# Optimization experiments

Hardware: AMD Instinct MI355X
Metric: run time of the kernel (lower is better)

The kernel has to match this reference:

```python
import jax, jax.numpy as jnp
import numpy as np

B, N, C = 32, 128, 128
HE = 64                      # n_hidden_edge
FILTERS = [64, 256, 512]
K = 3
NREL = 2
NH = 256                     # n_hidden
OUT = 10
EPS_BN = 1e-5


def _lin(key, fin, fout):
    return jax.random.normal(key, (fin, fout), jnp.float32) / np.sqrt(fin)


def setup_inputs() -> dict:
    key = jax.random.key(0)
    ks = iter(jax.random.split(key, 64))
    x = jax.random.normal(next(ks), (B, N, C), jnp.float32)
    # ragged mask: first n_b nodes active
    n_nodes = jax.random.randint(next(ks), (B,), 64, N + 1)
    mask = (jnp.arange(N)[None, :] < n_nodes[:, None]).astype(jnp.float32)
    A = jax.random.uniform(next(ks), (B, N, N), jnp.float32)
    A = A * mask[:, :, None] * mask[:, None, :]
    inp = {"x": x, "A": A, "mask": mask}
    # edge predictor MLP: Linear(2C,HE) -> ReLU -> Linear(HE,1)
    inp["eW1"] = _lin(next(ks), 2 * C, HE)
    inp["eb1"] = jnp.zeros((HE,), jnp.float32)
    inp["eW2"] = _lin(next(ks), HE, 1)
    inp["eb2"] = jnp.zeros((1,), jnp.float32)
    # 3 GraphConv layers: fc (in*K*NREL -> f), BN eval params
    fin = C
    for li, f in enumerate(FILTERS):
        inp[f"gW{li}"] = _lin(next(ks), fin * K * NREL, f)
        inp[f"gb{li}"] = jnp.zeros((f,), jnp.float32)
        inp[f"g{li}g"] = jnp.ones((f,), jnp.float32)
        inp[f"g{li}b"] = jnp.zeros((f,), jnp.float32)
        inp[f"g{li}m"] = 0.1 * jax.random.normal(next(ks), (f,), jnp.float32)
        inp[f"g{li}v"] = jax.random.uniform(next(ks), (f,), jnp.float32) + 0.5
        fin = f
    # classifier fc (dropout is identity in eval)
    inp["fW1"] = _lin(next(ks), FILTERS[-1], NH)
    inp["fb1"] = jnp.zeros((NH,), jnp.float32)
    inp["fW2"] = _lin(next(ks), NH, OUT)
    inp["fb2"] = jnp.zeros((OUT,), jnp.float32)
    return inp


def _edge_adjacency(x, mask, eW1, eb1, eW2, eb2):
    # edge_pred(cat(x_i,x_j)) for all pairs; flipped pass == transpose of scores
    u = x @ eW1[:C]          # [B,N,HE] (contribution of node i slot)
    v = x @ eW1[C:]          # [B,N,HE] (contribution of node j slot)
    h = jax.nn.relu(u[:, :, None, :] + v[:, None, :, :] + eb1)   # [B,N,N,HE]
    s = jnp.einsum('bijh,h->bij', h, eW2[:, 0]) + eb2[0]          # [B,N,N]
    y = jnp.exp(0.5 * (s + jnp.swapaxes(s, 1, 2)))
    # only masked upper-triangular pairs (i<j) were scattered in the original
    tri = jnp.triu(jnp.ones((N, N), bool), 1)
    pm = tri[None, :, :] * (mask[:, :, None] * mask[:, None, :])
    A_pred = y * pm
    rs = jnp.sum(A_pred, axis=2)                                 # row sums (torch sum over dim 1 of [N,N])
    rs = jnp.where(rs == 0.0, 1.0, rs)
    An = A_pred / rs[:, :, None]
    return An + jnp.swapaxes(An, 1, 2)


def _gconv(xh, A2, mask, W, b, g, be, m, v):
    outs = []
    for rel in range(A2.shape[-1]):
        Ar = A2[..., rel]
        # K>=2, scale_identity=False -> no identity added
        D = (jnp.sum(Ar, axis=1) + 1e-5) ** (-0.5)               # [B,N]
        L = D[:, :, None] * Ar * D[:, None, :]
        Xt = [xh, jnp.matmul(L, xh)]
        for _ in range(2, K):
            Xt.append(2.0 * jnp.matmul(L, Xt[-1]) - Xt[-2])
        outs.append(jnp.concatenate(Xt, axis=2))
    h = jnp.concatenate(outs, axis=2) @ W + b
    h = h * mask[:, :, None]
    h = (h - m) / jnp.sqrt(v + EPS_BN) * g + be                  # BatchNorm1d eval over channel dim
    return jax.nn.relu(h)


def reference(x, A, mask, eW1, eb1, eW2, eb2,
              gW0, gb0, g0g, g0b, g0m, g0v,
              gW1, gb1, g1g, g1b, g1m, g1v,
              gW2, gb2, g2g, g2b, g2m, g2v,
              fW1, fb1, fW2, fb2):
    An = _edge_adjacency(x, mask, eW1, eb1, eW2, eb2)
    A2 = jnp.stack((A, An), axis=3)                              # [B,N,N,2]
    h = _gconv(x, A2, mask, gW0, gb0, g0g, g0b, g0m, g0v)
    h = _gconv(h, A2, mask, gW1, gb1, g1g, g1b, g1m, g1v)
    h = _gconv(h, A2, mask, gW2, gb2, g2g, g2b, g2m, g2v)
    pooled = jnp.max(h, axis=1)                                  # [B, 512]
    # fc: Dropout(eval=id) -> Linear -> Dropout(eval=id) -> Linear (no activation)
    return (pooled @ fW1 + fb1) @ fW2 + fb2
```

## Files before the change

### kernel.cpp

```cpp
#include <hip/hip_runtime.h>

#define Bk 32
#define Nn 128
#define Cc 128
#define HE 64
#define BN_EPS 1e-5f

typedef __attribute__((ext_vector_type(8))) short short8;
typedef __attribute__((ext_vector_type(4))) float floatx4;

#define OFF_U    ((size_t)0)
#define OFF_V    ((size_t)262144)
#define OFF_S    ((size_t)524288)
#define OFF_AN   ((size_t)1048576)
#define OFF_LB   ((size_t)1572864)
#define OFF_H0   ((size_t)2097152)
#define OFF_H1   ((size_t)2359296)
#define OFF_H2   ((size_t)3407872)
#define OFF_XB   ((size_t)5505024)
#define OFF_WT   ((size_t)8650752)

__device__ __forceinline__ unsigned short f2b(float f) {
    unsigned int x = __float_as_uint(f);
    unsigned int r = x + 0x7FFFu + ((x >> 16) & 1u);
    return (unsigned short)(r >> 16);
}

__global__ __launch_bounds__(128) void edge_uv(const float* __restrict__ x,
                                               const float* __restrict__ eW1,
                                               const float* __restrict__ eb1,
                                               float* __restrict__ u, float* __restrict__ v) {
    int bn = blockIdx.x;
    int tid = threadIdx.x;
    __shared__ float xs[Cc];
    xs[tid] = x[(size_t)bn * Cc + tid];
    __syncthreads();
    int h = tid & 63;
    int which = tid >> 6;
    const float* W = eW1 + (size_t)which * Cc * HE + h;
    float acc = 0.f;
#pragma unroll 8
    for (int c = 0; c < Cc; ++c) acc += xs[c] * W[(size_t)c * HE];
    if (which == 0) u[(size_t)bn * HE + h] = acc + eb1[h];
    else            v[(size_t)bn * HE + h] = acc;
}

__global__ __launch_bounds__(256) void edge_score(const float* __restrict__ u,
                                                  const float* __restrict__ v,
                                                  const float* __restrict__ eW2,
                                                  const float* __restrict__ eb2,
                                                  float* __restrict__ s) {
    __shared__ float us[16][68], vs[16][68], w2[HE];
    int b = blockIdx.z;
    int i0 = blockIdx.y * 16, j0 = blockIdx.x * 16;
    int tid = threadIdx.x;
    int r = tid >> 4, c4 = (tid & 15) * 4;
    {
        const float4 uv = *(const float4*)(u + ((size_t)(b * Nn + i0 + r)) * HE + c4);
        us[r][c4] = uv.x; us[r][c4 + 1] = uv.y; us[r][c4 + 2] = uv.z; us[r][c4 + 3] = uv.w;
        const float4 vv = *(const float4*)(v + ((size_t)(b * Nn + j0 + r)) * HE + c4);
        vs[r][c4] = vv.x; vs[r][c4 + 1] = vv.y; vs[r][c4 + 2] = vv.z; vs[r][c4 + 3] = vv.w;
    }
    if (tid < HE) w2[tid] = eW2[tid];
    __syncthreads();
    int il = tid >> 4, jl = tid & 15;
    float acc = 0.f;
#pragma unroll
    for (int h = 0; h < HE; ++h) {
        float t = us[il][h] + vs[jl][h];
        acc += fmaxf(t, 0.f) * w2[h];
    }
    s[((size_t)(b * Nn + i0 + il)) * Nn + j0 + jl] = acc + eb2[0];
}

__global__ __launch_bounds__(256) void edge_apan(const float* __restrict__ s,
                                                 const float* __restrict__ mask,
                                                 float* __restrict__ An) {
    __shared__ float apS[128][129];
    __shared__ float rsS[128];
    __shared__ float msk[128];
    int b = blockIdx.x, tid = threadIdx.x;
    const float* sb = s + (size_t)b * Nn * Nn;
    if (tid < 128) msk[tid] = mask[b * Nn + tid];
    __syncthreads();
#pragma unroll
    for (int k = 0; k < 64; ++k) {
        int idx = tid + k * 256;
        int i = idx >> 7, j = idx & 127;
        float val = 0.f;
        if (j > i && msk[i] != 0.f && msk[j] != 0.f) {
            val = expf(fminf(0.5f * (sb[idx] + sb[j * Nn + i]), 80.f));
        }
        apS[i][j] = val;
    }
    __syncthreads();
    if (tid < 128) {
        float r = 0.f;
        for (int j = 0; j < 128; ++j) r += apS[tid][j];
        rsS[tid] = (r == 0.f) ? 1.f : r;
    }
    __syncthreads();
    float* Ab = An + (size_t)b * Nn * Nn;
#pragma unroll
    for (int k = 0; k < 64; ++k) {
        int idx = tid + k * 256;
        int i = idx >> 7, j = idx & 127;
        Ab[idx] = apS[i][j] / rsS[i] + apS[j][i] / rsS[j];
    }
}

__global__ __launch_bounds__(256) void buildLb(const float* __restrict__ A,
                                               const float* __restrict__ An,
                                               unsigned short* __restrict__ Lb) {
    int b = blockIdx.x & 31, rel = blockIdx.x >> 5;
    const float* Ar = (rel ? An : A) + (size_t)b * Nn * Nn;
    __shared__ float part[256];
    __shared__ float Ds[128];
    int tid = threadIdx.x;
    int j = tid & 127, half = tid >> 7;
    float sum = 0.f;
    for (int i = half * 64; i < half * 64 + 64; ++i) sum += Ar[i * Nn + j];
    part[tid] = sum;
    __syncthreads();
    if (tid < 128) Ds[tid] = rsqrtf(part[tid] + part[tid + 128] + 1e-5f);
    __syncthreads();
    unsigned short* Lo = Lb + ((size_t)(rel * Bk + b)) * Nn * Nn;
#pragma unroll
    for (int k = 0; k < 64; ++k) {
        int idx = tid + k * 256;
        int i = idx >> 7, jj = idx & 127;
        Lo[idx] = f2b(Ds[i] * Ar[idx] * Ds[jj]);
    }
}

__global__ __launch_bounds__(256) void prep_weights(const float* __restrict__ W0,
                                                    const float* __restrict__ W1,
                                                    const float* __restrict__ W2,
                                                    unsigned short* __restrict__ Wt) {
    int e = blockIdx.x * 256 + threadIdx.x;
    if (e < 49152) {
        int k = e >> 6, n = e & 63;
        Wt[n * 768 + k] = f2b(W0[e]);
        return;
    }
    e -= 49152;
    if (e < 98304) {
        int k = e >> 8, n = e & 255;
        Wt[49152 + n * 384 + k] = f2b(W1[e]);
        return;
    }
    e -= 98304;
    if (e < 786432) {
        int k = e >> 9, n = e & 511;
        Wt[147456 + n * 1536 + k] = f2b(W2[e]);
    }
}

template <int FIN>
__global__ __launch_bounds__(256) void cheb_fused(const unsigned short* __restrict__ Lb,
                                                  const float* __restrict__ xin,
                                                  unsigned short* __restrict__ Xb) {
    constexpr int LDK = 136;
    __shared__ __align__(16) unsigned short Ls[128 * LDK];
    __shared__ __align__(16) unsigned short XsT[64 * LDK];
    __shared__ __align__(16) unsigned short T1T[64 * LDK];
    int z = blockIdx.y;
    int b = z & 31, rel = z >> 5;
    int c0 = blockIdx.x * 64;
    int tid = threadIdx.x;
    int w = tid >> 6, lane = tid & 63, quad = lane >> 4, lr = lane & 15;
    const unsigned short* Lp = Lb + ((size_t)(rel * Bk + b)) * Nn * Nn;
    const float* Xp = xin + (size_t)b * Nn * FIN;
    const int ld6 = 6 * FIN;
    unsigned short* Xo = Xb + (size_t)b * Nn * ld6 + rel * 3 * FIN;

#pragma unroll
    for (int i = 0; i < 16; ++i) {
        int idx = tid + i * 256;
        int row = idx >> 5, col4 = (idx & 31) << 2;
        ushort4 val = *(const ushort4*)(Lp + row * Nn + col4);
        *(ushort4*)&Ls[row * LDK + col4] = val;
    }
    {
        int node = tid >> 1, cb = (tid & 1) * 32;
        const float* xr = Xp + (size_t)node * FIN + c0 + cb;
        unsigned short* t0w = Xo + (size_t)node * ld6 + c0 + cb;
#pragma unroll
        for (int i = 0; i < 8; ++i) {
            float4 vv = *(const float4*)(xr + i * 4);
            ushort4 o;
            o.x = f2b(vv.x); o.y = f2b(vv.y); o.z = f2b(vv.z); o.w = f2b(vv.w);
            *(ushort4*)(t0w + i * 4) = o;
            XsT[(cb + i * 4 + 0) * LDK + node] = o.x;
            XsT[(cb + i * 4 + 1) * LDK + node] = o.y;
            XsT[(cb + i * 4 + 2) * LDK + node] = o.z;
            XsT[(cb + i * 4 + 3) * LDK + node] = o.w;
        }
    }
    __syncthreads();

    floatx4 acc[2][4];
#pragma unroll
    for (int rt = 0; rt < 2; ++rt)
#pragma unroll
        for (int ct = 0; ct < 4; ++ct) acc[rt][ct] = (floatx4){0.f, 0.f, 0.f, 0.f};
#pragma unroll
    for (int kc = 0; kc < 4; ++kc) {
        short8 a[2], bb[4];
#pragma unroll
        for (int rt = 0; rt < 2; ++rt)
            a[rt] = *(const short8*)&Ls[((w * 2 + rt) * 16 + lr) * LDK + kc * 32 + quad * 8];
#pragma unroll
        for (int ct = 0; ct < 4; ++ct)
            bb[ct] = *(const short8*)&XsT[(ct * 16 + lr) * LDK + kc * 32 + quad * 8];
#pragma unroll
        for (int rt = 0; rt < 2; ++rt)
#pragma unroll
            for (int ct = 0; ct < 4; ++ct)
                acc[rt][ct] = __builtin_amdgcn_mfma_f32_16x16x32_bf16(a[rt], bb[ct], acc[rt][ct], 0, 0, 0);
    }
#pragma unroll
    for (int rt = 0; rt < 2; ++rt) {
        int rb = (w * 2 + rt) * 16 + quad * 4;
#pragma unroll
        for (int ct = 0; ct < 4; ++ct) {
            int col = ct * 16 + lr;
            ushort4 o;
            o.x = f2b(acc[rt][ct][0]); o.y = f2b(acc[rt][ct][1]);
            o.z = f2b(acc[rt][ct][2]); o.w = f2b(acc[rt][ct][3]);
            *(ushort4*)&T1T[col * LDK + rb] = o;
        }
    }
    __syncthreads();

    {
        int node = tid >> 1, cb = (tid & 1) * 32;
        unsigned short* t1w = Xo + (size_t)node * ld6 + FIN + c0 + cb;
#pragma unroll
        for (int i = 0; i < 8; ++i) {
            ushort4 o;
            o.x = T1T[(cb + i * 4 + 0) * LDK + node];
            o.y = T1T[(cb + i * 4 + 1) * LDK + node];
            o.z = T1T[(cb + i * 4 + 2) * LDK + node];
            o.w = T1T[(cb + i * 4 + 3) * LDK + node];
            *(ushort4*)(t1w + i * 4) = o;
        }
    }
    floatx4 acc2[2][4];
#pragma unroll
    for (int rt = 0; rt < 2; ++rt)
#pragma unroll
        for (int ct = 0; ct < 4; ++ct) acc2[rt][ct] = (floatx4){0.f, 0.f, 0.f, 0.f};
#pragma unroll
    for (int kc = 0; kc < 4; ++kc) {
        short8 a[2], bb[4];
#pragma unroll
        for (int rt = 0; rt < 2; ++rt)
            a[rt] = *(const short8*)&Ls[((w * 2 + rt) * 16 + lr) * LDK + kc * 32 + quad * 8];
#pragma unroll
        for (int ct = 0; ct < 4; ++ct)
            bb[ct] = *(const short8*)&T1T[(ct * 16 + lr) * LDK + kc * 32 + quad * 8];
#pragma unroll
        for (int rt = 0; rt < 2; ++rt)
#pragma unroll
            for (int ct = 0; ct < 4; ++ct)
                acc2[rt][ct] = __builtin_amdgcn_mfma_f32_16x16x32_bf16(a[rt], bb[ct], acc2[rt][ct], 0, 0, 0);
    }
#pragma unroll
    for (int rt = 0; rt < 2; ++rt) {
        int rb = (w * 2 + rt) * 16 + quad * 4;
#pragma unroll
        for (int ct = 0; ct < 4; ++ct) {
            int col = ct * 16 + lr;
            ushort4 o;
            float t0a = Xp[(size_t)(rb + 0) * FIN + c0 + col];
            float t0b = Xp[(size_t)(rb + 1) * FIN + c0 + col];
            float t0c = Xp[(size_t)(rb + 2) * FIN + c0 + col];
            float t0d = Xp[(size_t)(rb + 3) * FIN + c0 + col];
            o.x = f2b(2.f * acc2[rt][ct][0] - t0a);
            o.y = f2b(2.f * acc2[rt][ct][1] - t0b);
            o.z = f2b(2.f * acc2[rt][ct][2] - t0c);
            o.w = f2b(2.f * acc2[rt][ct][3] - t0d);
            *(ushort4*)&XsT[col * LDK + rb] = o;
        }
    }
    __syncthreads();
    {
        int node = tid >> 1, cb = (tid & 1) * 32;
        unsigned short* t2w = Xo + (size_t)node * ld6 + 2 * FIN + c0 + cb;
#pragma unroll
        for (int i = 0; i < 8; ++i) {
            ushort4 o;
            o.x = XsT[(cb + i * 4 + 0) * LDK + node];
            o.y = XsT[(cb + i * 4 + 1) * LDK + node];
            o.z = XsT[(cb + i * 4 + 2) * LDK + node];
            o.w = XsT[(cb + i * 4 + 3) * LDK + node];
            *(ushort4*)(t2w + i * 4) = o;
        }
    }
}

template <int RT>
__global__ __launch_bounds__(256) void fc_mfma(const unsigned short* __restrict__ Xb,
                                               const unsigned short* __restrict__ Wt,
                                               const float* __restrict__ bias,
                                               const float* __restrict__ mask,
                                               const float* __restrict__ bnG,
                                               const float* __restrict__ bnB,
                                               const float* __restrict__ bnM,
                                               const float* __restrict__ bnV,
                                               float* __restrict__ out, int Kd, int F) {
    __shared__ __align__(16) unsigned short As[RT * 64 * 40];
    __shared__ __align__(16) unsigned short Bs[64 * 40];
    int tid = threadIdx.x;
    int w = tid >> 6, lane = tid & 63, quad = lane >> 4, lr = lane & 15;
    int row0 = blockIdx.y * (RT * 64), col0 = blockIdx.x * 64;

    floatx4 acc[RT][4];
#pragma unroll
    for (int rt = 0; rt < RT; ++rt)
#pragma unroll
        for (int ct = 0; ct < 4; ++ct) acc[rt][ct] = (floatx4){0.f, 0.f, 0.f, 0.f};

    int arow[RT], asub[RT];
#pragma unroll
    for (int i = 0; i < RT; ++i) { int ch = tid + i * 256; arow[i] = ch >> 2; asub[i] = ch & 3; }
    int brow = tid >> 2, bsub = tid & 3;

    for (int k0 = 0; k0 < Kd; k0 += 32) {
        short8 ra[RT];
#pragma unroll
        for (int i = 0; i < RT; ++i)
            ra[i] = *(const short8*)(Xb + (size_t)(row0 + arow[i]) * Kd + k0 + asub[i] * 8);
        short8 rb = *(const short8*)(Wt + (size_t)(col0 + brow) * Kd + k0 + bsub * 8);
        __syncthreads();
#pragma unroll
        for (int i = 0; i < RT; ++i)
            *(short8*)&As[arow[i] * 40 + asub[i] * 8] = ra[i];
        *(short8*)&Bs[brow * 40 + bsub * 8] = rb;
        __syncthreads();
        short8 a[RT], b[4];
#pragma unroll
        for (int rt = 0; rt < RT; ++rt)
            a[rt] = *(const short8*)&As[(w * RT * 16 + rt * 16 + lr) * 40 + quad * 8];
#pragma unroll
        for (int ct = 0; ct < 4; ++ct)
            b[ct] = *(const short8*)&Bs[(ct * 16 + lr) * 40 + quad * 8];
#pragma unroll
        for (int rt = 0; rt < RT; ++rt)
#pragma unroll
            for (int ct = 0; ct < 4; ++ct)
                acc[rt][ct] = __builtin_amdgcn_mfma_f32_16x16x32_bf16(a[rt], b[ct], acc[rt][ct], 0, 0, 0);
    }

#pragma unroll
    for (int rt = 0; rt < RT; ++rt) {
        int rbase = row0 + w * RT * 16 + rt * 16 + quad * 4;
#pragma unroll
        for (int ct = 0; ct < 4; ++ct) {
            int col = col0 + ct * 16 + lr;
            float bi = bias[col];
            float sc = rsqrtf(bnV[col] + BN_EPS) * bnG[col];
            float bm = bnM[col], bb = bnB[col];
#pragma unroll
            for (int reg = 0; reg < 4; ++reg) {
                int row = rbase + reg;
                float h = acc[rt][ct][reg] + bi;
                h *= mask[row];
                h = (h - bm) * sc + bb;
                out[(size_t)row * F + col] = fmaxf(h, 0.f);
            }
        }
    }
}

__global__ __launch_bounds__(256) void pool_cls(const float* __restrict__ h2,
                                                const float* __restrict__ fW1,
                                                const float* __restrict__ fb1,
                                                const float* __restrict__ fW2,
                                                const float* __restrict__ fb2,
                                                float* __restrict__ out) {
    int b = blockIdx.x;
    int tid = threadIdx.x;
    __shared__ float ps[512], hs[256];
    const float* p = h2 + (size_t)b * Nn * 512;
    float m1 = p[tid], m2 = p[tid + 256];
    for (int n = 1; n < Nn; ++n) {
        m1 = fmaxf(m1, p[(size_t)n * 512 + tid]);
        m2 = fmaxf(m2, p[(size_t)n * 512 + tid + 256]);
    }
    ps[tid] = m1;
    ps[tid + 256] = m2;
    __syncthreads();
    float acc = fb1[tid];
    for (int c = 0; c < 512; ++c) acc += ps[c] * fW1[(size_t)c * 256 + tid];
    hs[tid] = acc;
    __syncthreads();
    if (tid < 10) {
        float o = fb2[tid];
        for (int h = 0; h < 256; ++h) o += hs[h] * fW2[(size_t)h * 10 + tid];
        out[(size_t)b * 10 + tid] = o;
    }
}

extern "C" void kernel_launch(void* const* d_in, const int* in_sizes, int n_in,
                              void* d_out, int out_size, void* d_ws, size_t ws_size,
                              hipStream_t stream) {
    const float* x    = (const float*)d_in[0];
    const float* Ain  = (const float*)d_in[1];
    const float* mask = (const float*)d_in[2];
    const float* eW1  = (const float*)d_in[3];
    const float* eb1  = (const float*)d_in[4];
    const float* eW2  = (const float*)d_in[5];
    const float* eb2  = (const float*)d_in[6];
    const float* fW1  = (const float*)d_in[25];
    const float* fb1  = (const float*)d_in[26];
    const float* fW2  = (const float*)d_in[27];
    const float* fb2  = (const float*)d_in[28];

    float* ws = (float*)d_ws;
    float* u  = ws + OFF_U;
    float* v  = ws + OFF_V;
    float* s  = ws + OFF_S;
    float* An = ws + OFF_AN;
    unsigned short* Lb = (unsigned short*)(ws + OFF_LB);
    float* h0 = ws + OFF_H0;
    float* h1 = ws + OFF_H1;
    float* h2 = ws + OFF_H2;
    unsigned short* Xb = (unsigned short*)(ws + OFF_XB);
    unsigned short* Wt = (unsigned short*)(ws + OFF_WT);

    prep_weights<<<3648, 256, 0, stream>>>((const float*)d_in[7], (const float*)d_in[13],
                                           (const float*)d_in[19], Wt);

    edge_uv<<<Bk * Nn, 128, 0, stream>>>(x, eW1, eb1, u, v);
    edge_score<<<dim3(8, 8, Bk), 256, 0, stream>>>(u, v, eW2, eb2, s);
    edge_apan<<<Bk, 256, 0, stream>>>(s, mask, An);

    buildLb<<<Bk * 2, 256, 0, stream>>>(Ain, An, Lb);

    const float* xins[3] = {x, h0, h1};
    float* houts[3] = {h0, h1, h2};
    const unsigned short* Wts[3] = {Wt, Wt + 49152, Wt + 147456};
    const int Kds[3] = {768, 384, 1536};
    const int fouts[3] = {64, 256, 512};
    for (int li = 0; li < 3; ++li) {
        int base = 7 + li * 6;
        const float* gb = (const float*)d_in[base + 1];
        const float* gg = (const float*)d_in[base + 2];
        const float* gB = (const float*)d_in[base + 3];
        const float* gm = (const float*)d_in[base + 4];
        const float* gv = (const float*)d_in[base + 5];

        if (li == 0)      cheb_fused<128><<<dim3(2, 64), 256, 0, stream>>>(Lb, xins[li], Xb);
        else if (li == 1) cheb_fused<64><<<dim3(1, 64), 256, 0, stream>>>(Lb, xins[li], Xb);
        else              cheb_fused<256><<<dim3(4, 64), 256, 0, stream>>>(Lb, xins[li], Xb);

        if (li == 0)
            fc_mfma<1><<<dim3(fouts[li] / 64, 64), 256, 0, stream>>>(
                Xb, Wts[li], gb, mask, gg, gB, gm, gv, houts[li], Kds[li], fouts[li]);
        else
            fc_mfma<2><<<dim3(fouts[li] / 64, 32), 256, 0, stream>>>(
                Xb, Wts[li], gb, mask, gg, gB, gm, gv, houts[li], Kds[li], fouts[li]);
    }

    pool_cls<<<Bk, 256, 0, stream>>>(h2, fW1, fb1, fW2, fb2, (float*)d_out);
}
```

Measured before the change: 286.4 us.

## Fuse edge Laplacian build, pool into FC epilogue, MFMA edge projection, fold classifier

```diff
diff --git a/kernel.cpp b/kernel.cpp
--- a/kernel.cpp
+++ b/kernel.cpp
@@ -9,16 +9,18 @@
 typedef __attribute__((ext_vector_type(8))) short short8;
 typedef __attribute__((ext_vector_type(4))) float floatx4;
 
-#define OFF_U    ((size_t)0)
-#define OFF_V    ((size_t)262144)
+#define OFF_UV   ((size_t)0)
 #define OFF_S    ((size_t)524288)
-#define OFF_AN   ((size_t)1048576)
-#define OFF_LB   ((size_t)1572864)
-#define OFF_H0   ((size_t)2097152)
-#define OFF_H1   ((size_t)2359296)
-#define OFF_H2   ((size_t)3407872)
-#define OFF_XB   ((size_t)5505024)
-#define OFF_WT   ((size_t)8650752)
+#define OFF_LB   ((size_t)1048576)
+#define OFF_H0   ((size_t)1572864)
+#define OFF_H1   ((size_t)1835008)
+#define OFF_POOL ((size_t)2883584)
+#define OFF_WC   ((size_t)2899968)
+#define OFF_BC   ((size_t)2905088)
+#define OFF_XB0  ((size_t)2905104)
+#define OFF_XB   ((size_t)3167248)
+#define OFF_WT   ((size_t)6312976)
+#define WUV_OFS  933888
 
 __device__ __forceinline__ unsigned short f2b(float f) {
     unsigned int x = __float_as_uint(f);
@@ -26,94 +28,209 @@
     return (unsigned short)(r >> 16);
 }
 
-__global__ __launch_bounds__(128) void edge_uv(const float* __restrict__ x,
-                                               const float* __restrict__ eW1,
+__global__ __launch_bounds__(256) void prep_all(const float* __restrict__ W0,
+                                                const float* __restrict__ W1,
+                                                const float* __restrict__ W2,
+                                                const float* __restrict__ eW1,
+                                                const float* __restrict__ fW1,
+                                                const float* __restrict__ fb1,
+                                                const float* __restrict__ fW2,
+                                                const float* __restrict__ fb2,
+                                                const float* __restrict__ x,
+                                                unsigned short* __restrict__ Wt,
+                                                float* __restrict__ Wc,
+                                                float* __restrict__ bc,
+                                                unsigned short* __restrict__ xb0) {
+    __shared__ unsigned short Ts[64][65];
+    int bid = blockIdx.x, tid = threadIdx.x;
+    if (bid < 228) {
+        const float* src; unsigned short* dst; int N, ldK, k0, n0;
+        if (bid < 12)      { src = W0; dst = Wt;          N = 64;  ldK = 768;  k0 = bid * 64;        n0 = 0; }
+        else if (bid < 36) { int t = bid - 12; src = W1; dst = Wt + 49152;  N = 256; ldK = 384;  k0 = (t % 6) * 64;  n0 = (t / 6) * 64; }
+        else               { int t = bid - 36; src = W2; dst = Wt + 147456; N = 512; ldK = 1536; k0 = (t % 24) * 64; n0 = (t / 24) * 64; }
+#pragma unroll
+        for (int p = 0; p < 16; ++p) {
+            int e = tid + p * 256; int r = e >> 6, c = e & 63;
+            Ts[r][c] = f2b(src[(size_t)(k0 + r) * N + n0 + c]);
+        }
+        __syncthreads();
+#pragma unroll
+        for (int p = 0; p < 16; ++p) {
+            int e = tid + p * 256; int n = e >> 6, k = e & 63;
+            dst[(size_t)(n0 + n) * ldK + k0 + k] = Ts[k][n];
+        }
+        return;
+    }
+    if (bid < 232) {
+        int tt = bid - 228;
+        int half = tt >> 1, kt = tt & 1;
+        int k0 = kt * 64;
+        unsigned short* Wuv = Wt + WUV_OFS;
+#pragma unroll
+        for (int p = 0; p < 16; ++p) {
+            int e = tid + p * 256; int r = e >> 6, c = e & 63;
+            Ts[r][c] = f2b(eW1[(size_t)(half * 128 + k0 + r) * 64 + c]);
+        }
+        __syncthreads();
+#pragma unroll
+        for (int p = 0; p < 16; ++p) {
+            int e = tid + p * 256; int n = e >> 6, k = e & 63;
+            Wuv[(size_t)(half * 64 + n) * 128 + k0 + k] = Ts[k][n];
+        }
+        return;
+    }
+    if (bid < 253) {
+        int e = (bid - 232) * 256 + tid;
+        if (e < 5120) {
+            int i = e / 10, j = e - i * 10;
+            float acc = 0.f;
+            for (int h = 0; h < 256; ++h) acc += fW1[(size_t)i * 256 + h] * fW2[(size_t)h * 10 + j];
+            Wc[e] = acc;
+        } else if (e < 5130) {
+            int j = e - 5120;
+            float acc = fb2[j];
+            for (int h = 0; h < 256; ++h) acc += fb1[h] * fW2[(size_t)h * 10 + j];
+            bc[j] = acc;
+        }
+        return;
+    }
+    {
+        int idx = (bid - 253) * 256 + tid;
+        float4 vv = ((const float4*)x)[idx];
+        ushort4 o;
+        o.x = f2b(vv.x); o.y = f2b(vv.y); o.z = f2b(vv.z); o.w = f2b(vv.w);
+        ((ushort4*)xb0)[idx] = o;
+    }
+}
+
+__global__ __launch_bounds__(256) void uv_mfma(const unsigned short* __restrict__ xb0,
+                                               const unsigned short* __restrict__ Wuv,
                                                const float* __restrict__ eb1,
-                                               float* __restrict__ u, float* __restrict__ v) {
-    int bn = blockIdx.x;
+                                               float* __restrict__ uv) {
+    __shared__ __align__(16) unsigned short As[128 * 40];
+    __shared__ __align__(16) unsigned short Bs[64 * 40];
     int tid = threadIdx.x;
-    __shared__ float xs[Cc];
-    xs[tid] = x[(size_t)bn * Cc + tid];
-    __syncthreads();
-    int h = tid & 63;
-    int which = tid >> 6;
-    const float* W = eW1 + (size_t)which * Cc * HE + h;
-    float acc = 0.f;
-#pragma unroll 8
-    for (int c = 0; c < Cc; ++c) acc += xs[c] * W[(size_t)c * HE];
-    if (which == 0) u[(size_t)bn * HE + h] = acc + eb1[h];
-    else            v[(size_t)bn * HE + h] = acc;
-}
-
-__global__ __launch_bounds__(256) void edge_score(const float* __restrict__ u,
-                                                  const float* __restrict__ v,
+    int w = tid >> 6, lane = tid & 63, quad = lane >> 4, lr = lane & 15;
+    int row0 = blockIdx.y * 128, col0 = blockIdx.x * 64;
+    floatx4 acc[2][4];
+#pragma unroll
+    for (int rt = 0; rt < 2; ++rt)
+#pragma unroll
+        for (int ct = 0; ct < 4; ++ct) acc[rt][ct] = (floatx4){0.f, 0.f, 0.f, 0.f};
+    int arow[2], asub[2];
+#pragma unroll
+    for (int i = 0; i < 2; ++i) { int ch = tid + i * 256; arow[i] = ch >> 2; asub[i] = ch & 3; }
+    int brow = tid >> 2, bsub = tid & 3;
+    for (int k0 = 0; k0 < 128; k0 += 32) {
+        short8 ra[2];
+#pragma unroll
+        for (int i = 0; i < 2; ++i)
+            ra[i] = *(const short8*)(xb0 + (size_t)(row0 + arow[i]) * 128 + k0 + asub[i] * 8);
+        short8 rb = *(const short8*)(Wuv + (size_t)(col0 + brow) * 128 + k0 + bsub * 8);
+        __syncthreads();
+#pragma unroll
+        for (int i = 0; i < 2; ++i) *(short8*)&As[arow[i] * 40 + asub[i] * 8] = ra[i];
+        *(short8*)&Bs[brow * 40 + bsub * 8] = rb;
+        __syncthreads();
+        short8 a[2], b[4];
+#pragma unroll
+        for (int rt = 0; rt < 2; ++rt)
+            a[rt] = *(const short8*)&As[(w * 32 + rt * 16 + lr) * 40 + quad * 8];
+#pragma unroll
+        for (int ct = 0; ct < 4; ++ct)
+            b[ct] = *(const short8*)&Bs[(ct * 16 + lr) * 40 + quad * 8];
+#pragma unroll
+        for (int rt = 0; rt < 2; ++rt)
+#pragma unroll
+            for (int ct = 0; ct < 4; ++ct)
+                acc[rt][ct] = __builtin_amdgcn_mfma_f32_16x16x32_bf16(a[rt], b[ct], acc[rt][ct], 0, 0, 0);
+    }
+#pragma unroll
+    for (int rt = 0; rt < 2; ++rt) {
+        int rbase = row0 + w * 32 + rt * 16 + quad * 4;
+#pragma unroll
+        for (int ct = 0; ct < 4; ++ct) {
+            int col = col0 + ct * 16 + lr;
+            float bi = (col < 64) ? eb1[col] : 0.f;
+#pragma unroll
+            for (int reg = 0; reg < 4; ++reg)
+                uv[(size_t)(rbase + reg) * 128 + col] = acc[rt][ct][reg] + bi;
+        }
+    }
+}
+
+__global__ __launch_bounds__(256) void edge_score(const float* __restrict__ uv,
                                                   const float* __restrict__ eW2,
                                                   const float* __restrict__ eb2,
                                                   float* __restrict__ s) {
-    __shared__ float us[16][68], vs[16][68], w2[HE];
+    __shared__ __align__(16) float us[16][76];
+    __shared__ __align__(16) float vs[16][76];
+    __shared__ __align__(16) float w2[64];
     int b = blockIdx.z;
     int i0 = blockIdx.y * 16, j0 = blockIdx.x * 16;
     int tid = threadIdx.x;
     int r = tid >> 4, c4 = (tid & 15) * 4;
-    {
-        const float4 uv = *(const float4*)(u + ((size_t)(b * Nn + i0 + r)) * HE + c4);
-        us[r][c4] = uv.x; us[r][c4 + 1] = uv.y; us[r][c4 + 2] = uv.z; us[r][c4 + 3] = uv.w;
-        const float4 vv = *(const float4*)(v + ((size_t)(b * Nn + j0 + r)) * HE + c4);
-        vs[r][c4] = vv.x; vs[r][c4 + 1] = vv.y; vs[r][c4 + 2] = vv.z; vs[r][c4 + 3] = vv.w;
-    }
-    if (tid < HE) w2[tid] = eW2[tid];
+    *(float4*)&us[r][c4] = *(const float4*)(uv + ((size_t)(b * Nn + i0 + r)) * 128 + c4);
+    *(float4*)&vs[r][c4] = *(const float4*)(uv + ((size_t)(b * Nn + j0 + r)) * 128 + 64 + c4);
+    if (tid < 64) w2[tid] = eW2[tid];
     __syncthreads();
     int il = tid >> 4, jl = tid & 15;
     float acc = 0.f;
 #pragma unroll
-    for (int h = 0; h < HE; ++h) {
-        float t = us[il][h] + vs[jl][h];
-        acc += fmaxf(t, 0.f) * w2[h];
+    for (int h4 = 0; h4 < 16; ++h4) {
+        float4 uu = *(const float4*)&us[il][h4 * 4];
+        float4 vv = *(const float4*)&vs[jl][h4 * 4];
+        float4 ww = *(const float4*)&w2[h4 * 4];
+        acc += fmaxf(uu.x + vv.x, 0.f) * ww.x + fmaxf(uu.y + vv.y, 0.f) * ww.y
+             + fmaxf(uu.z + vv.z, 0.f) * ww.z + fmaxf(uu.w + vv.w, 0.f) * ww.w;
     }
     s[((size_t)(b * Nn + i0 + il)) * Nn + j0 + jl] = acc + eb2[0];
 }
 
-__global__ __launch_bounds__(256) void edge_apan(const float* __restrict__ s,
-                                                 const float* __restrict__ mask,
-                                                 float* __restrict__ An) {
+__global__ __launch_bounds__(256) void edge_apanL(const float* __restrict__ s,
+                                                  const float* __restrict__ mask,
+                                                  unsigned short* __restrict__ Lb) {
     __shared__ float apS[128][129];
-    __shared__ float rsS[128];
-    __shared__ float msk[128];
+    __shared__ float msk[128], invS[128], t1S[128], Dv[128];
     int b = blockIdx.x, tid = threadIdx.x;
     const float* sb = s + (size_t)b * Nn * Nn;
     if (tid < 128) msk[tid] = mask[b * Nn + tid];
     __syncthreads();
-#pragma unroll
     for (int k = 0; k < 64; ++k) {
         int idx = tid + k * 256;
         int i = idx >> 7, j = idx & 127;
         float val = 0.f;
-        if (j > i && msk[i] != 0.f && msk[j] != 0.f) {
+        if (j > i && msk[i] != 0.f && msk[j] != 0.f)
             val = expf(fminf(0.5f * (sb[idx] + sb[j * Nn + i]), 80.f));
-        }
         apS[i][j] = val;
     }
     __syncthreads();
     if (tid < 128) {
         float r = 0.f;
         for (int j = 0; j < 128; ++j) r += apS[tid][j];
-        rsS[tid] = (r == 0.f) ? 1.f : r;
-    }
-    __syncthreads();
-    float* Ab = An + (size_t)b * Nn * Nn;
-#pragma unroll
+        invS[tid] = (r == 0.f) ? 1.f : (1.f / r);
+        t1S[tid] = (r == 0.f) ? 0.f : 1.f;
+    }
+    __syncthreads();
+    if (tid < 128) {
+        float cw = 0.f;
+        for (int j = 0; j < 128; ++j) cw += apS[j][tid] * invS[j];
+        Dv[tid] = rsqrtf(t1S[tid] + cw + 1e-5f);
+    }
+    __syncthreads();
+    unsigned short* Lo = Lb + ((size_t)(Bk + b)) * Nn * Nn;
     for (int k = 0; k < 64; ++k) {
         int idx = tid + k * 256;
         int i = idx >> 7, j = idx & 127;
-        Ab[idx] = apS[i][j] / rsS[i] + apS[j][i] / rsS[j];
-    }
-}
-
-__global__ __launch_bounds__(256) void buildLb(const float* __restrict__ A,
-                                               const float* __restrict__ An,
-                                               unsigned short* __restrict__ Lb) {
-    int b = blockIdx.x & 31, rel = blockIdx.x >> 5;
-    const float* Ar = (rel ? An : A) + (size_t)b * Nn * Nn;
+        float an = apS[i][j] * invS[i] + apS[j][i] * invS[j];
+        Lo[idx] = f2b(Dv[i] * an * Dv[j]);
+    }
+}
+
+__global__ __launch_bounds__(256) void buildLb_A(const float* __restrict__ A,
+                                                 unsigned short* __restrict__ Lb) {
+    int b = blockIdx.x;
+    const float* Ar = A + (size_t)b * Nn * Nn;
     __shared__ float part[256];
     __shared__ float Ds[128];
     int tid = threadIdx.x;
@@ -124,35 +241,11 @@
     __syncthreads();
     if (tid < 128) Ds[tid] = rsqrtf(part[tid] + part[tid + 128] + 1e-5f);
     __syncthreads();
-    unsigned short* Lo = Lb + ((size_t)(rel * Bk + b)) * Nn * Nn;
-#pragma unroll
+    unsigned short* Lo = Lb + (size_t)b * Nn * Nn;
     for (int k = 0; k < 64; ++k) {
         int idx = tid + k * 256;
         int i = idx >> 7, jj = idx & 127;
         Lo[idx] = f2b(Ds[i] * Ar[idx] * Ds[jj]);
-    }
-}
-
-__global__ __launch_bounds__(256) void prep_weights(const float* __restrict__ W0,
-                                                    const float* __restrict__ W1,
-                                                    const float* __restrict__ W2,
-                                                    unsigned short* __restrict__ Wt) {
-    int e = blockIdx.x * 256 + threadIdx.x;
-    if (e < 49152) {
-        int k = e >> 6, n = e & 63;
-        Wt[n * 768 + k] = f2b(W0[e]);
-        return;
-    }
-    e -= 49152;
-    if (e < 98304) {
-        int k = e >> 8, n = e & 255;
-        Wt[49152 + n * 384 + k] = f2b(W1[e]);
-        return;
-    }
-    e -= 98304;
-    if (e < 786432) {
-        int k = e >> 9, n = e & 511;
-        Wt[147456 + n * 1536 + k] = f2b(W2[e]);
     }
 }
 
@@ -232,7 +325,6 @@
         }
     }
     __syncthreads();
-
     {
         int node = tid >> 1, cb = (tid & 1) * 32;
         unsigned short* t1w = Xo + (size_t)node * ld6 + FIN + c0 + cb;
@@ -300,7 +392,7 @@
     }
 }
 
-template <int RT>
+template <int RT, bool POOL>
 __global__ __launch_bounds__(256) void fc_mfma(const unsigned short* __restrict__ Xb,
                                                const unsigned short* __restrict__ Wt,
                                                const float* __restrict__ bias,
@@ -309,9 +401,12 @@
                                                const float* __restrict__ bnB,
                                                const float* __restrict__ bnM,
                                                const float* __restrict__ bnV,
-                                               float* __restrict__ out, int Kd, int F) {
+                                               float* __restrict__ out,
+                                               float* __restrict__ pooled,
+                                               int Kd, int F) {
     __shared__ __align__(16) unsigned short As[RT * 64 * 40];
     __shared__ __align__(16) unsigned short Bs[64 * 40];
+    __shared__ float wmax[4][64];
     int tid = threadIdx.x;
     int w = tid >> 6, lane = tid & 63, quad = lane >> 4, lr = lane & 15;
     int row0 = blockIdx.y * (RT * 64), col0 = blockIdx.x * 64;
@@ -353,6 +448,7 @@
                 acc[rt][ct] = __builtin_amdgcn_mfma_f32_16x16x32_bf16(a[rt], b[ct], acc[rt][ct], 0, 0, 0);
     }
 
+    float cm[4] = {0.f, 0.f, 0.f, 0.f};
 #pragma unroll
     for (int rt = 0; rt < RT; ++rt) {
         int rbase = row0 + w * RT * 16 + rt * 16 + quad * 4;
@@ -368,38 +464,48 @@
                 float h = acc[rt][ct][reg] + bi;
                 h *= mask[row];
                 h = (h - bm) * sc + bb;
-                out[(size_t)row * F + col] = fmaxf(h, 0.f);
+                h = fmaxf(h, 0.f);
+                if (POOL) cm[ct] = fmaxf(cm[ct], h);
+                else      out[(size_t)row * F + col] = h;
             }
         }
     }
-}
-
-__global__ __launch_bounds__(256) void pool_cls(const float* __restrict__ h2,
-                                                const float* __restrict__ fW1,
-                                                const float* __restrict__ fb1,
-                                                const float* __restrict__ fW2,
-                                                const float* __restrict__ fb2,
-                                                float* __restrict__ out) {
-    int b = blockIdx.x;
-    int tid = threadIdx.x;
-    __shared__ float ps[512], hs[256];
-    const float* p = h2 + (size_t)b * Nn * 512;
-    float m1 = p[tid], m2 = p[tid + 256];
-    for (int n = 1; n < Nn; ++n) {
-        m1 = fmaxf(m1, p[(size_t)n * 512 + tid]);
-        m2 = fmaxf(m2, p[(size_t)n * 512 + tid + 256]);
-    }
-    ps[tid] = m1;
-    ps[tid + 256] = m2;
-    __syncthreads();
-    float acc = fb1[tid];
-    for (int c = 0; c < 512; ++c) acc += ps[c] * fW1[(size_t)c * 256 + tid];
-    hs[tid] = acc;
+    if (POOL) {
+#pragma unroll
+        for (int ct = 0; ct < 4; ++ct) {
+            cm[ct] = fmaxf(cm[ct], __shfl_xor(cm[ct], 16));
+            cm[ct] = fmaxf(cm[ct], __shfl_xor(cm[ct], 32));
+            if (quad == 0) wmax[w][ct * 16 + lr] = cm[ct];
+        }
+        __syncthreads();
+        if (tid < 64) {
+            float g = fmaxf(fmaxf(wmax[0][tid], wmax[1][tid]), fmaxf(wmax[2][tid], wmax[3][tid]));
+            int b = blockIdx.y;
+            pooled[(size_t)b * 512 + col0 + tid] = g;
+        }
+    }
+}
+
+__global__ __launch_bounds__(256) void cls_final(const float* __restrict__ pooled,
+                                                 const float* __restrict__ Wc,
+                                                 const float* __restrict__ bc,
+                                                 float* __restrict__ out) {
+    __shared__ float red[16][17];
+    int b = blockIdx.x, tid = threadIdx.x;
+    int o = tid & 15, slice = tid >> 4;
+    float p = 0.f;
+    if (o < 10) {
+        for (int kk = 0; kk < 32; ++kk) {
+            int k = slice * 32 + kk;
+            p += pooled[(size_t)b * 512 + k] * Wc[(size_t)k * 10 + o];
+        }
+    }
+    red[slice][o] = p;
     __syncthreads();
     if (tid < 10) {
-        float o = fb2[tid];
-        for (int h = 0; h < 256; ++h) o += hs[h] * fW2[(size_t)h * 10 + tid];
-        out[(size_t)b * 10 + tid] = o;
+        float sum = bc[tid];
+        for (int sli = 0; sli < 16; ++sli) sum += red[sli][tid];
+        out[(size_t)b * 10 + tid] = sum;
     }
 }
 
@@ -419,31 +525,30 @@
     const float* fb2  = (const float*)d_in[28];
 
     float* ws = (float*)d_ws;
-    float* u  = ws + OFF_U;
-    float* v  = ws + OFF_V;
+    float* uv = ws + OFF_UV;
     float* s  = ws + OFF_S;
-    float* An = ws + OFF_AN;
     unsigned short* Lb = (unsigned short*)(ws + OFF_LB);
     float* h0 = ws + OFF_H0;
     float* h1 = ws + OFF_H1;
-    float* h2 = ws + OFF_H2;
-    unsigned short* Xb = (unsigned short*)(ws + OFF_XB);
-    unsigned short* Wt = (unsigned short*)(ws + OFF_WT);
-
-    prep_weights<<<3648, 256, 0, stream>>>((const float*)d_in[7], (const float*)d_in[13],
-                                           (const float*)d_in[19], Wt);
-
-    edge_uv<<<Bk * Nn, 128, 0, stream>>>(x, eW1, eb1, u, v);
-    edge_score<<<dim3(8, 8, Bk), 256, 0, stream>>>(u, v, eW2, eb2, s);
-    edge_apan<<<Bk, 256, 0, stream>>>(s, mask, An);
-
-    buildLb<<<Bk * 2, 256, 0, stream>>>(Ain, An, Lb);
+    float* pl = ws + OFF_POOL;
+    float* Wc = ws + OFF_WC;
+    float* bc = ws + OFF_BC;
+    unsigned short* xb0 = (unsigned short*)(ws + OFF_XB0);
+    unsigned short* Xb  = (unsigned short*)(ws + OFF_XB);
+    unsigned short* Wt  = (unsigned short*)(ws + OFF_WT);
+
+    prep_all<<<765, 256, 0, stream>>>((const float*)d_in[7], (const float*)d_in[13],
+                                      (const float*)d_in[19], eW1, fW1, fb1, fW2, fb2, x,
+                                      Wt, Wc, bc, xb0);
+
+    uv_mfma<<<dim3(2, 32), 256, 0, stream>>>(xb0, Wt + WUV_OFS, eb1, uv);
+    edge_score<<<dim3(8, 8, Bk), 256, 0, stream>>>(uv, eW2, eb2, s);
+    edge_apanL<<<Bk, 256, 0, stream>>>(s, mask, Lb);
+    buildLb_A<<<Bk, 256, 0, stream>>>(Ain, Lb);
 
     const float* xins[3] = {x, h0, h1};
-    float* houts[3] = {h0, h1, h2};
     const unsigned short* Wts[3] = {Wt, Wt + 49152, Wt + 147456};
     const int Kds[3] = {768, 384, 1536};
-    const int fouts[3] = {64, 256, 512};
     for (int li = 0; li < 3; ++li) {
         int base = 7 + li * 6;
         const float* gb = (const float*)d_in[base + 1];
@@ -457,12 +562,15 @@
         else              cheb_fused<256><<<dim3(4, 64), 256, 0, stream>>>(Lb, xins[li], Xb);
 
         if (li == 0)
-            fc_mfma<1><<<dim3(fouts[li] / 64, 64), 256, 0, stream>>>(
-                Xb, Wts[li], gb, mask, gg, gB, gm, gv, houts[li], Kds[li], fouts[li]);
+            fc_mfma<1, false><<<dim3(1, 64), 256, 0, stream>>>(
+                Xb, Wts[li], gb, mask, gg, gB, gm, gv, h0, nullptr, Kds[li], 64);
+        else if (li == 1)
+            fc_mfma<2, false><<<dim3(4, 32), 256, 0, stream>>>(
+                Xb, Wts[li], gb, mask, gg, gB, gm, gv, h1, nullptr, Kds[li], 256);
         else
-            fc_mfma<2><<<dim3(fouts[li] / 64, 32), 256, 0, stream>>>(
-                Xb, Wts[li], gb, mask, gg, gB, gm, gv, houts[li], Kds[li], fouts[li]);
-    }
-
-    pool_cls<<<Bk, 256, 0, stream>>>(h2, fW1, fb1, fW2, fb2, (float*)d_out);
-}
+            fc_mfma<2, true><<<dim3(8, 32), 256, 0, stream>>>(
+                Xb, Wts[li], gb, mask, gg, gB, gm, gv, nullptr, pl, Kds[li], 512);
+    }
+
+    cls_final<<<Bk, 256, 0, stream>>>(pl, Wc, bc, (float*)d_out);
+}
```

Result: faster. 269.2 us (-6.0%).
